# Optimization experiments

Measured on AMD Instinct MI355X. Metric: run time of the kernel, lower is better.

Reference implementation:

```python
import jax, jax.numpy as jnp
import numpy as np

C = 256
C8 = C // 8


def setup_inputs() -> dict:
    key = jax.random.key(0)
    ks = jax.random.split(key, 9)
    B, H, W = 4, 64, 64
    inp = jax.random.normal(ks[0], (B, C, H, W), dtype=jnp.float32)
    original = jax.random.normal(ks[1], (B, C, H, W), dtype=jnp.float32)
    s = 1.0 / np.sqrt(C)
    wq = jax.random.normal(ks[2], (C8, C), dtype=jnp.float32) * s
    bq = jax.random.normal(ks[3], (C8,), dtype=jnp.float32) * 0.01
    wk = jax.random.normal(ks[4], (C8, C), dtype=jnp.float32) * s
    bk = jax.random.normal(ks[5], (C8,), dtype=jnp.float32) * 0.01
    wv = jax.random.normal(ks[6], (C, C), dtype=jnp.float32) * s
    bv = jax.random.normal(ks[7], (C,), dtype=jnp.float32) * 0.01
    # torch inits gamma to 0; use a nonzero value so the attention branch contributes
    gamma = jnp.asarray([0.5], dtype=jnp.float32)
    return {"input": inp, "original": original, "wq": wq, "bq": bq,
            "wk": wk, "bk": bk, "wv": wv, "bv": bv, "gamma": gamma}


def reference(input, original, wq, bq, wk, bk, wv, bv, gamma):
    B, Cc, H, W = input.shape
    HW = H * W
    x = input.reshape(B, Cc, HW)          # [B, C, HW]
    o = original.reshape(B, Cc, HW)
    # 1x1 convs == per-pixel linear projections
    q = jnp.einsum('oc,bcn->bno', wq, x) + bq          # [B, HW, C8]
    k = jnp.einsum('oc,bcn->bon', wk, x) + bk[:, None]  # [B, C8, HW]
    v = jnp.einsum('oc,bcn->bon', wv, o) + bv[:, None]  # [B, C, HW]
    attn = jax.nn.softmax(jnp.einsum('bic,bcj->bij', q, k), axis=-1)  # [B, HW, HW]
    out = jnp.einsum('bcj,bij->bci', v, attn)           # [B, C, HW]
    out = out.reshape(B, Cc, H, W)
    return gamma[0] * out + input
```

## Files before the change

kernel.cpp:

```cpp
#include <hip/hip_runtime.h>

typedef short s16x8 __attribute__((ext_vector_type(8)));
typedef float f32x4 __attribute__((ext_vector_type(4)));
typedef float f32x16 __attribute__((ext_vector_type(16)));

#define B_ 4
#define C_ 256
#define S_ 4096
#define LOG2E 1.44269504088896f
#define M2 32.0f

#if __has_builtin(__builtin_amdgcn_exp2f)
#define EXP2(x) __builtin_amdgcn_exp2f(x)
#else
#define EXP2(x) __exp2f(x)
#endif

__device__ __forceinline__ unsigned short f2b(float f) {
  union { float f; unsigned u; } v; v.f = f;
  unsigned r = v.u + 0x7fffu + ((v.u >> 16) & 1u);
  return (unsigned short)(r >> 16);
}
__device__ __forceinline__ unsigned short f2b_fast(float f) {
  union { float f; unsigned u; } v; v.f = f;
  return (unsigned short)((v.u + 0x8000u) >> 16);
}
__device__ __forceinline__ s16x8 lds_ld8(const unsigned short* p) {
  union { s16x8 v; uint2 u[2]; } r;
  r.u[0] = *(const uint2*)p;
  r.u[1] = *(const uint2*)(p + 4);
  return r.v;
}

__global__ __launch_bounds__(256)
void proj_kernel(const float* __restrict__ x, const float* __restrict__ orig,
                 const float* __restrict__ wq, const float* __restrict__ bq,
                 const float* __restrict__ wk, const float* __restrict__ bk,
                 const float* __restrict__ wv, const float* __restrict__ bv,
                 unsigned short* __restrict__ Qb, unsigned short* __restrict__ Kb,
                 unsigned short* __restrict__ Vf) {
  __shared__ unsigned short Al[64 * 68];
  __shared__ unsigned short Sl[64 * 68];
  const int ct = blockIdx.x >> 6;
  const int jt = blockIdx.x & 63;
  const int n0 = jt * 64;
  const int b  = blockIdx.y;
  const int t  = threadIdx.x;
  const int L = t & 63, w = t >> 6;
  const int mt = w >> 1, nt = w & 1;
  const int g = L >> 5, l32 = L & 31;
  const float* srcb = ((ct == 0) ? x : orig) + (size_t)b * C_ * S_;
  f32x16 acc = (f32x16)0.0f;

  for (int kc = 0; kc < 4; ++kc) {
    const int k0 = kc * 64;
    __syncthreads();
    #pragma unroll
    for (int rep = 0; rep < 4; ++rep) {
      const int idx = rep * 256 + t;
      const int row = idx >> 4, c4 = (idx & 15) * 4;
      const float* wsrc; int wrow;
      if (ct == 0) {
        if (row < 32) { wsrc = wq; wrow = row; } else { wsrc = wk; wrow = row - 32; }
      } else { wsrc = wv; wrow = (ct - 1) * 64 + row; }
      f32x4 v = *(const f32x4*)(wsrc + (size_t)wrow * 256 + k0 + c4);
      union { unsigned short us[4]; uint2 u2; } pk;
      #pragma unroll
      for (int i = 0; i < 4; ++i) pk.us[i] = f2b(v[i]);
      *(uint2*)&Al[row * 68 + c4] = pk.u2;
    }
    {
      const int c4 = (t >> 4) * 4;
      const int n4 = (t & 15) * 4;
      f32x4 v0 = *(const f32x4*)(srcb + (size_t)(k0 + c4 + 0) * S_ + n0 + n4);
      f32x4 v1 = *(const f32x4*)(srcb + (size_t)(k0 + c4 + 1) * S_ + n0 + n4);
      f32x4 v2 = *(const f32x4*)(srcb + (size_t)(k0 + c4 + 2) * S_ + n0 + n4);
      f32x4 v3 = *(const f32x4*)(srcb + (size_t)(k0 + c4 + 3) * S_ + n0 + n4);
      #pragma unroll
      for (int k = 0; k < 4; ++k) {
        union { unsigned short us[4]; uint2 u2; } pk;
        pk.us[0] = f2b(v0[k]); pk.us[1] = f2b(v1[k]);
        pk.us[2] = f2b(v2[k]); pk.us[3] = f2b(v3[k]);
        *(uint2*)&Sl[(n4 + k) * 68 + c4] = pk.u2;
      }
    }
    __syncthreads();
    #pragma unroll
    for (int ks = 0; ks < 4; ++ks) {
      s16x8 af = lds_ld8(&Al[(mt * 32 + l32) * 68 + ks * 16 + g * 8]);
      s16x8 bf = lds_ld8(&Sl[(nt * 32 + l32) * 68 + ks * 16 + g * 8]);
      acc = __builtin_amdgcn_mfma_f32_32x32x16_bf16(af, bf, acc, 0, 0, 0);
    }
  }
  __syncthreads();
  unsigned short* Rl = Al;
  const int n = nt * 32 + l32;
  if (ct == 0) {
    #pragma unroll
    for (int reg = 0; reg < 16; ++reg) {
      const int rr = (reg & 3) + 8 * (reg >> 2) + 4 * g;
      const float val = (mt == 0) ? (acc[reg] + bq[rr]) * LOG2E : acc[reg] + bk[rr];
      Rl[n * 68 + mt * 32 + rr] = f2b(val);
    }
    __syncthreads();
    const int nn = t >> 2, ch0 = (t & 3) * 16;
    s16x8 a = lds_ld8(Rl + nn * 68 + ch0);
    s16x8 c = lds_ld8(Rl + nn * 68 + ch0 + 8);
    unsigned short* dst = (ch0 < 32)
        ? Qb + ((size_t)b * S_ + n0 + nn) * 32 + ch0
        : Kb + ((size_t)b * S_ + n0 + nn) * 32 + (ch0 - 32);
    *(s16x8*)dst = a;
    *(s16x8*)(dst + 8) = c;
  } else {
    const int cg = ct - 1;
    #pragma unroll
    for (int reg = 0; reg < 16; ++reg) {
      const int rr = (reg & 3) + 8 * (reg >> 2) + 4 * g;
      const int ch = mt * 32 + rr;
      Rl[ch * 68 + n] = f2b(acc[reg] + bv[cg * 64 + ch]);
    }
    __syncthreads();
    unsigned short* grp = Vf + ((size_t)(b * 64 + jt) * 4 + cg) * 4096;
    #pragma unroll
    for (int k = 0; k < 2; ++k) {
      const int G = t * 2 + k;
      const int vv = G >> 8, kb = (G >> 6) & 3, Lf = G & 63;
      const int ch64 = vv * 32 + (Lf & 31);
      const int j64  = kb * 16 + (Lf >> 5) * 8;
      s16x8 v = lds_ld8(Rl + ch64 * 68 + j64);
      *(s16x8*)(grp + G * 8) = v;
    }
  }
}

union FlashU {
  unsigned short P[64 * 68];
  float scr[128][66];
};

__global__ __launch_bounds__(512, 4)
void flash_kernel(const unsigned short* __restrict__ Qb,
                  const unsigned short* __restrict__ Kb,
                  const unsigned short* __restrict__ Vf,
                  const float* __restrict__ inp,
                  const float* __restrict__ gamma,
                  float* __restrict__ out) {
  __shared__ FlashU sm;
  __shared__ float lpart[2][64];
  __shared__ float invl[64];
  const int l   = blockIdx.x;
  const int b   = (l & 7) >> 1;
  const int chh = (l >> 3) & 1;
  const int i0  = ((l >> 4) * 2 + (l & 1)) * 64;
  const int t  = threadIdx.x;
  const int L = t & 63, w = t >> 6;
  const int q4 = L >> 4, c16 = L & 15;
  const int g  = L >> 5, l32 = L & 31;
  const int rh = w & 3, jh = w >> 2;
  const int cq = w & 3, ih = w >> 2;
  const float gam = gamma[0];
  const unsigned short* Kbase = Kb + (size_t)b * S_ * 32;
  const s16x8 qf = *(const s16x8*)(Qb + ((size_t)b * S_ + i0 + rh * 16 + c16) * 32 + q4 * 8);

  const int vcg = chh * 2 + (cq >> 1);
  const int vvv = cq & 1;

  f32x16 acc = (f32x16)0.0f;
  float lp[4] = {0.f, 0.f, 0.f, 0.f};

  s16x8 kc0 = *(const s16x8*)(Kbase + (size_t)(c16) * 32 + q4 * 8 + (size_t)(jh * 32) * 32);
  s16x8 kc1 = *(const s16x8*)(Kbase + (size_t)(jh * 32 + 16 + c16) * 32 + q4 * 8);

  for (int j0 = 0; j0 < S_; j0 += 64) {
    const int jt = j0 >> 6;
    const int jn = (j0 + 64 < S_) ? j0 + 64 : j0;
    s16x8 kn0 = *(const s16x8*)(Kbase + (size_t)(jn + jh * 32 + c16) * 32 + q4 * 8);
    s16x8 kn1 = *(const s16x8*)(Kbase + (size_t)(jn + jh * 32 + 16 + c16) * 32 + q4 * 8);
    const unsigned short* vb = Vf + ((size_t)(b * 64 + jt) * 4 + vcg) * 4096 + vvv * 2048;
    s16x8 vf0 = *(const s16x8*)(vb + 0 * 512 + L * 8);
    s16x8 vf1 = *(const s16x8*)(vb + 1 * 512 + L * 8);
    s16x8 vf2 = *(const s16x8*)(vb + 2 * 512 + L * 8);
    s16x8 vf3 = *(const s16x8*)(vb + 3 * 512 + L * 8);
    f32x4 cinit = (f32x4)(-M2);
    f32x4 s0 = __builtin_amdgcn_mfma_f32_16x16x32_bf16(qf, kc0, cinit, 0, 0, 0);
    f32x4 s1 = __builtin_amdgcn_mfma_f32_16x16x32_bf16(qf, kc1, cinit, 0, 0, 0);
    #pragma unroll
    for (int r = 0; r < 4; ++r) {
      const float p0 = EXP2(s0[r]);
      const float p1 = EXP2(s1[r]);
      lp[r] += p0 + p1;
      const int row = rh * 16 + q4 * 4 + r;
      sm.P[row * 68 + jh * 32 + c16]      = f2b_fast(p0);
      sm.P[row * 68 + jh * 32 + 16 + c16] = f2b_fast(p1);
    }
    __syncthreads();
    {
      s16x8 pf;
      pf = lds_ld8(sm.P + (ih * 32 + l32) * 68 + 0 * 16 + g * 8);
      acc = __builtin_amdgcn_mfma_f32_32x32x16_bf16(pf, vf0, acc, 0, 0, 0);
      pf = lds_ld8(sm.P + (ih * 32 + l32) * 68 + 1 * 16 + g * 8);
      acc = __builtin_amdgcn_mfma_f32_32x32x16_bf16(pf, vf1, acc, 0, 0, 0);
      pf = lds_ld8(sm.P + (ih * 32 + l32) * 68 + 2 * 16 + g * 8);
      acc = __builtin_amdgcn_mfma_f32_32x32x16_bf16(pf, vf2, acc, 0, 0, 0);
      pf = lds_ld8(sm.P + (ih * 32 + l32) * 68 + 3 * 16 + g * 8);
      acc = __builtin_amdgcn_mfma_f32_32x32x16_bf16(pf, vf3, acc, 0, 0, 0);
    }
    __syncthreads();
    kc0 = kn0; kc1 = kn1;
  }
  #pragma unroll
  for (int r = 0; r < 4; ++r) {
    float v = lp[r];
    #pragma unroll
    for (int d = 1; d < 16; d <<= 1) v += __shfl_xor(v, d, 64);
    lp[r] = v;
  }
  if (c16 == 0) {
    #pragma unroll
    for (int r = 0; r < 4; ++r) lpart[jh][rh * 16 + q4 * 4 + r] = lp[r];
  }
  __syncthreads();
  if (t < 64) invl[t] = gam / (lpart[0][t] + lpart[1][t]);
  #pragma unroll
  for (int reg = 0; reg < 16; ++reg) {
    const int rr = (reg & 3) + 8 * (reg >> 2) + 4 * g;
    sm.scr[cq * 32 + l32][ih * 32 + rr] = acc[reg];
  }
  __syncthreads();
  {
    const int ch = t >> 2;
    const int ic = (t & 3) * 16;
    #pragma unroll
    for (int q = 0; q < 4; ++q) {
      const int il = ic + q * 4;
      const size_t gi = ((size_t)b * C_ + chh * 128 + ch) * S_ + i0 + il;
      const f32x4 iv = *(const f32x4*)(inp + gi);
      f32x4 o;
      #pragma unroll
      for (int k = 0; k < 4; ++k)
        o[k] = sm.scr[ch][il + k] * invl[il + k] + iv[k];
      *(f32x4*)(out + gi) = o;
    }
  }
}

extern "C" void kernel_launch(void* const* d_in, const int* in_sizes, int n_in,
                              void* d_out, int out_size, void* d_ws, size_t ws_size,
                              hipStream_t stream) {
  const float* inp   = (const float*)d_in[0];
  const float* orig  = (const float*)d_in[1];
  const float* wq    = (const float*)d_in[2];
  const float* bq    = (const float*)d_in[3];
  const float* wk    = (const float*)d_in[4];
  const float* bk    = (const float*)d_in[5];
  const float* wv    = (const float*)d_in[6];
  const float* bv    = (const float*)d_in[7];
  const float* gamma = (const float*)d_in[8];
  float* out = (float*)d_out;

  unsigned short* Qb = (unsigned short*)d_ws;
  unsigned short* Kb = Qb + (size_t)B_ * S_ * 32;
  unsigned short* Vf = Kb + (size_t)B_ * S_ * 32;

  proj_kernel<<<dim3(320, 4), 256, 0, stream>>>(inp, orig, wq, bq, wk, bk, wv, bv, Qb, Kb, Vf);
  flash_kernel<<<512, 512, 0, stream>>>(Qb, Kb, Vf, inp, gamma, out);
}
```

Baseline: 168.4 us.

## Double-buffer P tile and software-pipeline flash loop with transposed score MFMA

The flash attention loop now uses two P buffers in LDS and is unrolled by two, so the exp/score phase of the next tile overlaps the PV MFMA of the current tile. This cuts the syncs per tile from two to one. The score MFMA operands are swapped (K as A, Q as B), so each lane holds four consecutive columns of one row. That allows packed 8-byte LDS stores and a single scalar row-sum reduced with two shuffles instead of sixteen. K/V loads are prefetched one tile further ahead, which raises register pressure and doubles P LDS usage.

```diff
diff --git a/kernel.cpp b/kernel.cpp
--- a/kernel.cpp
+++ b/kernel.cpp
@@ -134,9 +134,56 @@
 }
 
 union FlashU {
-  unsigned short P[64 * 68];
+  unsigned short P[2][64 * 68];
   float scr[128][66];
 };
+
+#define PHASE_A(PBUF, K0, K1)                                                   \
+  {                                                                             \
+    f32x4 cinit = (f32x4)(-M2);                                                 \
+    f32x4 s0 = __builtin_amdgcn_mfma_f32_16x16x32_bf16(K0, qf, cinit, 0, 0, 0); \
+    f32x4 s1 = __builtin_amdgcn_mfma_f32_16x16x32_bf16(K1, qf, cinit, 0, 0, 0); \
+    const float p0a = EXP2(s0[0]), p0b = EXP2(s0[1]);                           \
+    const float p0c = EXP2(s0[2]), p0d = EXP2(s0[3]);                           \
+    const float p1a = EXP2(s1[0]), p1b = EXP2(s1[1]);                           \
+    const float p1c = EXP2(s1[2]), p1d = EXP2(s1[3]);                           \
+    lpv += ((p0a + p0b) + (p0c + p0d)) + ((p1a + p1b) + (p1c + p1d));           \
+    uint2 w0, w1;                                                               \
+    w0.x = (unsigned)f2b_fast(p0a) | ((unsigned)f2b_fast(p0b) << 16);           \
+    w0.y = (unsigned)f2b_fast(p0c) | ((unsigned)f2b_fast(p0d) << 16);           \
+    w1.x = (unsigned)f2b_fast(p1a) | ((unsigned)f2b_fast(p1b) << 16);          \
+    w1.y = (unsigned)f2b_fast(p1c) | ((unsigned)f2b_fast(p1d) << 16);          \
+    unsigned short* pw = sm.P[PBUF] + prow_off;                                 \
+    *(uint2*)(pw)      = w0;                                                    \
+    *(uint2*)(pw + 16) = w1;                                                    \
+  }
+
+#define PHASE_B(PBUF, V0, V1, V2, V3)                                           \
+  {                                                                             \
+    s16x8 pf;                                                                   \
+    pf = lds_ld8(sm.P[PBUF] + pread_off + 0 * 16);                              \
+    acc = __builtin_amdgcn_mfma_f32_32x32x16_bf16(pf, V0, acc, 0, 0, 0);        \
+    pf = lds_ld8(sm.P[PBUF] + pread_off + 1 * 16);                              \
+    acc = __builtin_amdgcn_mfma_f32_32x32x16_bf16(pf, V1, acc, 0, 0, 0);        \
+    pf = lds_ld8(sm.P[PBUF] + pread_off + 2 * 16);                              \
+    acc = __builtin_amdgcn_mfma_f32_32x32x16_bf16(pf, V2, acc, 0, 0, 0);        \
+    pf = lds_ld8(sm.P[PBUF] + pread_off + 3 * 16);                              \
+    acc = __builtin_amdgcn_mfma_f32_32x32x16_bf16(pf, V3, acc, 0, 0, 0);        \
+  }
+
+#define LOAD_K(JT, K0, K1)                                                          \
+  K0 = *(const s16x8*)(Kbase + (size_t)((JT) * 64 + jh * 32 + c16) * 32 + q4 * 8);  \
+  K1 = *(const s16x8*)(Kbase + (size_t)((JT) * 64 + jh * 32 + 16 + c16) * 32 + q4 * 8);
+
+#define LOAD_V(JT, V0, V1, V2, V3)                                             \
+  {                                                                            \
+    const unsigned short* vb = Vf + ((size_t)(b * 64 + (JT)) * 4 + vcg) * 4096 \
+                               + vvv * 2048 + L * 8;                           \
+    V0 = *(const s16x8*)(vb + 0 * 512);                                        \
+    V1 = *(const s16x8*)(vb + 1 * 512);                                        \
+    V2 = *(const s16x8*)(vb + 2 * 512);                                        \
+    V3 = *(const s16x8*)(vb + 3 * 512);                                        \
+  }
 
 __global__ __launch_bounds__(512, 4)
 void flash_kernel(const unsigned short* __restrict__ Qb,
@@ -165,60 +212,35 @@
   const int vcg = chh * 2 + (cq >> 1);
   const int vvv = cq & 1;
 
+  const int prow_off  = (rh * 16 + c16) * 68 + jh * 32 + q4 * 4;
+  const int pread_off = (ih * 32 + l32) * 68 + g * 8;
+
   f32x16 acc = (f32x16)0.0f;
-  float lp[4] = {0.f, 0.f, 0.f, 0.f};
-
-  s16x8 kc0 = *(const s16x8*)(Kbase + (size_t)(c16) * 32 + q4 * 8 + (size_t)(jh * 32) * 32);
-  s16x8 kc1 = *(const s16x8*)(Kbase + (size_t)(jh * 32 + 16 + c16) * 32 + q4 * 8);
-
-  for (int j0 = 0; j0 < S_; j0 += 64) {
-    const int jt = j0 >> 6;
-    const int jn = (j0 + 64 < S_) ? j0 + 64 : j0;
-    s16x8 kn0 = *(const s16x8*)(Kbase + (size_t)(jn + jh * 32 + c16) * 32 + q4 * 8);
-    s16x8 kn1 = *(const s16x8*)(Kbase + (size_t)(jn + jh * 32 + 16 + c16) * 32 + q4 * 8);
-    const unsigned short* vb = Vf + ((size_t)(b * 64 + jt) * 4 + vcg) * 4096 + vvv * 2048;
-    s16x8 vf0 = *(const s16x8*)(vb + 0 * 512 + L * 8);
-    s16x8 vf1 = *(const s16x8*)(vb + 1 * 512 + L * 8);
-    s16x8 vf2 = *(const s16x8*)(vb + 2 * 512 + L * 8);
-    s16x8 vf3 = *(const s16x8*)(vb + 3 * 512 + L * 8);
-    f32x4 cinit = (f32x4)(-M2);
-    f32x4 s0 = __builtin_amdgcn_mfma_f32_16x16x32_bf16(qf, kc0, cinit, 0, 0, 0);
-    f32x4 s1 = __builtin_amdgcn_mfma_f32_16x16x32_bf16(qf, kc1, cinit, 0, 0, 0);
-    #pragma unroll
-    for (int r = 0; r < 4; ++r) {
-      const float p0 = EXP2(s0[r]);
-      const float p1 = EXP2(s1[r]);
-      lp[r] += p0 + p1;
-      const int row = rh * 16 + q4 * 4 + r;
-      sm.P[row * 68 + jh * 32 + c16]      = f2b_fast(p0);
-      sm.P[row * 68 + jh * 32 + 16 + c16] = f2b_fast(p1);
-    }
+  float lpv = 0.f;
+
+  s16x8 kE0, kE1, kO0, kO1;
+  s16x8 vE0, vE1, vE2, vE3, vO0, vO1, vO2, vO3;
+  LOAD_K(0, kE0, kE1);
+  LOAD_V(0, vE0, vE1, vE2, vE3);
+
+  for (int jt = 0; jt < 64; jt += 2) {
+    PHASE_A(0, kE0, kE1);
+    __syncthreads();
+    LOAD_K(jt + 1, kO0, kO1);
+    LOAD_V(jt + 1, vO0, vO1, vO2, vO3);
+    PHASE_B(0, vE0, vE1, vE2, vE3);
+    PHASE_A(1, kO0, kO1);
     __syncthreads();
     {
-      s16x8 pf;
-      pf = lds_ld8(sm.P + (ih * 32 + l32) * 68 + 0 * 16 + g * 8);
-      acc = __builtin_amdgcn_mfma_f32_32x32x16_bf16(pf, vf0, acc, 0, 0, 0);
-      pf = lds_ld8(sm.P + (ih * 32 + l32) * 68 + 1 * 16 + g * 8);
-      acc = __builtin_amdgcn_mfma_f32_32x32x16_bf16(pf, vf1, acc, 0, 0, 0);
-      pf = lds_ld8(sm.P + (ih * 32 + l32) * 68 + 2 * 16 + g * 8);
-      acc = __builtin_amdgcn_mfma_f32_32x32x16_bf16(pf, vf2, acc, 0, 0, 0);
-      pf = lds_ld8(sm.P + (ih * 32 + l32) * 68 + 3 * 16 + g * 8);
-      acc = __builtin_amdgcn_mfma_f32_32x32x16_bf16(pf, vf3, acc, 0, 0, 0);
-    }
-    __syncthreads();
-    kc0 = kn0; kc1 = kn1;
-  }
-  #pragma unroll
-  for (int r = 0; r < 4; ++r) {
-    float v = lp[r];
-    #pragma unroll
-    for (int d = 1; d < 16; d <<= 1) v += __shfl_xor(v, d, 64);
-    lp[r] = v;
-  }
-  if (c16 == 0) {
-    #pragma unroll
-    for (int r = 0; r < 4; ++r) lpart[jh][rh * 16 + q4 * 4 + r] = lp[r];
-  }
+      const int jn = (jt + 2 < 64) ? jt + 2 : 62;
+      LOAD_K(jn, kE0, kE1);
+      LOAD_V(jn, vE0, vE1, vE2, vE3);
+    }
+    PHASE_B(1, vO0, vO1, vO2, vO3);
+  }
+  lpv += __shfl_xor(lpv, 16, 64);
+  lpv += __shfl_xor(lpv, 32, 64);
+  if (L < 16) lpart[jh][rh * 16 + L] = lpv;
   __syncthreads();
   if (t < 64) invl[t] = gam / (lpart[0][t] + lpart[1][t]);
   #pragma unroll
```

Measured after the change: 172.8 us. 2.6% more time.

## Double-buffer P tile, process 128 keys per step with swapped QK operands

Applied to the files above, without the earlier changes.

The flash loop now handles 128 keys per iteration and ping-pongs between two P buffers in LDS. This cuts the barriers per key block from two to one and overlaps the PV MFMAs of one half with the softmax of the other. The QK MFMA operands are swapped so each lane owns one query row. That lets P be written as packed 4-element vector stores and the row-sum reduction drop to two shuffles. Two independent accumulators break the MFMA dependency chain, at the cost of more registers for K and V prefetches, which risks spills or lower occupancy under launch_bounds(512,4).

```diff
diff --git a/kernel.cpp b/kernel.cpp
--- a/kernel.cpp
+++ b/kernel.cpp
@@ -133,10 +133,79 @@
   }
 }
 
+#define PSTR 132
+
 union FlashU {
-  unsigned short P[64 * 68];
+  unsigned short P[2][64 * PSTR];
   float scr[128][66];
 };
+
+#define PACK4(S, DST)                                                           \
+  {                                                                             \
+    const float p0 = EXP2((S)[0]), p1 = EXP2((S)[1]);                           \
+    const float p2 = EXP2((S)[2]), p3 = EXP2((S)[3]);                           \
+    lpv += (p0 + p1) + (p2 + p3);                                               \
+    uint2 wv_;                                                                  \
+    wv_.x = (unsigned)f2b_fast(p0) | ((unsigned)f2b_fast(p1) << 16);            \
+    wv_.y = (unsigned)f2b_fast(p2) | ((unsigned)f2b_fast(p3) << 16);            \
+    *(uint2*)(DST) = wv_;                                                       \
+  }
+
+#define PHASE_A2(PBUF, KA, KB, KC, KD)                                          \
+  {                                                                             \
+    const f32x4 cinit = (f32x4)(-M2);                                           \
+    f32x4 s0 = __builtin_amdgcn_mfma_f32_16x16x32_bf16(KA, qf, cinit, 0, 0, 0); \
+    f32x4 s1 = __builtin_amdgcn_mfma_f32_16x16x32_bf16(KB, qf, cinit, 0, 0, 0); \
+    f32x4 s2 = __builtin_amdgcn_mfma_f32_16x16x32_bf16(KC, qf, cinit, 0, 0, 0); \
+    f32x4 s3 = __builtin_amdgcn_mfma_f32_16x16x32_bf16(KD, qf, cinit, 0, 0, 0); \
+    unsigned short* pw = sm.P[PBUF] + prowA;                                    \
+    PACK4(s0, pw);                                                              \
+    PACK4(s1, pw + 16);                                                         \
+    PACK4(s2, pw + 32);                                                         \
+    PACK4(s3, pw + 48);                                                         \
+  }
+
+#define PHASE_B2(PBUF)                                                          \
+  {                                                                             \
+    s16x8 pf;                                                                   \
+    pf = lds_ld8(sm.P[PBUF] + preadB + 0 * 16);                                 \
+    accA = __builtin_amdgcn_mfma_f32_32x32x16_bf16(pf, v0, accA, 0, 0, 0);      \
+    pf = lds_ld8(sm.P[PBUF] + preadB + 4 * 16);                                 \
+    accB = __builtin_amdgcn_mfma_f32_32x32x16_bf16(pf, v4, accB, 0, 0, 0);      \
+    pf = lds_ld8(sm.P[PBUF] + preadB + 1 * 16);                                 \
+    accA = __builtin_amdgcn_mfma_f32_32x32x16_bf16(pf, v1, accA, 0, 0, 0);      \
+    pf = lds_ld8(sm.P[PBUF] + preadB + 5 * 16);                                 \
+    accB = __builtin_amdgcn_mfma_f32_32x32x16_bf16(pf, v5, accB, 0, 0, 0);      \
+    pf = lds_ld8(sm.P[PBUF] + preadB + 2 * 16);                                 \
+    accA = __builtin_amdgcn_mfma_f32_32x32x16_bf16(pf, v2, accA, 0, 0, 0);      \
+    pf = lds_ld8(sm.P[PBUF] + preadB + 6 * 16);                                 \
+    accB = __builtin_amdgcn_mfma_f32_32x32x16_bf16(pf, v6, accB, 0, 0, 0);      \
+    pf = lds_ld8(sm.P[PBUF] + preadB + 3 * 16);                                 \
+    accA = __builtin_amdgcn_mfma_f32_32x32x16_bf16(pf, v3, accA, 0, 0, 0);      \
+    pf = lds_ld8(sm.P[PBUF] + preadB + 7 * 16);                                 \
+    accB = __builtin_amdgcn_mfma_f32_32x32x16_bf16(pf, v7, accB, 0, 0, 0);      \
+  }
+
+#define LOAD_K2(IU, KA, KB, KC, KD)                                                      \
+  KA = *(const s16x8*)(Kbase + (size_t)((IU) * 128 + jh * 64 +  0 + c16) * 32 + q4 * 8); \
+  KB = *(const s16x8*)(Kbase + (size_t)((IU) * 128 + jh * 64 + 16 + c16) * 32 + q4 * 8); \
+  KC = *(const s16x8*)(Kbase + (size_t)((IU) * 128 + jh * 64 + 32 + c16) * 32 + q4 * 8); \
+  KD = *(const s16x8*)(Kbase + (size_t)((IU) * 128 + jh * 64 + 48 + c16) * 32 + q4 * 8);
+
+#define LOAD_V2(IU)                                                                  \
+  {                                                                                  \
+    const unsigned short* vb0 = Vf + ((size_t)(b * 64 + (IU) * 2) * 4 + vcg) * 4096  \
+                                + vvv * 2048 + L * 8;                                \
+    v0 = *(const s16x8*)(vb0 + 0 * 512);                                             \
+    v1 = *(const s16x8*)(vb0 + 1 * 512);                                             \
+    v2 = *(const s16x8*)(vb0 + 2 * 512);                                             \
+    v3 = *(const s16x8*)(vb0 + 3 * 512);                                             \
+    const unsigned short* vb1 = vb0 + 4 * 4096;                                      \
+    v4 = *(const s16x8*)(vb1 + 0 * 512);                                             \
+    v5 = *(const s16x8*)(vb1 + 1 * 512);                                             \
+    v6 = *(const s16x8*)(vb1 + 2 * 512);                                             \
+    v7 = *(const s16x8*)(vb1 + 3 * 512);                                             \
+  }
 
 __global__ __launch_bounds__(512, 4)
 void flash_kernel(const unsigned short* __restrict__ Qb,
@@ -165,66 +234,44 @@
   const int vcg = chh * 2 + (cq >> 1);
   const int vvv = cq & 1;
 
-  f32x16 acc = (f32x16)0.0f;
-  float lp[4] = {0.f, 0.f, 0.f, 0.f};
-
-  s16x8 kc0 = *(const s16x8*)(Kbase + (size_t)(c16) * 32 + q4 * 8 + (size_t)(jh * 32) * 32);
-  s16x8 kc1 = *(const s16x8*)(Kbase + (size_t)(jh * 32 + 16 + c16) * 32 + q4 * 8);
-
-  for (int j0 = 0; j0 < S_; j0 += 64) {
-    const int jt = j0 >> 6;
-    const int jn = (j0 + 64 < S_) ? j0 + 64 : j0;
-    s16x8 kn0 = *(const s16x8*)(Kbase + (size_t)(jn + jh * 32 + c16) * 32 + q4 * 8);
-    s16x8 kn1 = *(const s16x8*)(Kbase + (size_t)(jn + jh * 32 + 16 + c16) * 32 + q4 * 8);
-    const unsigned short* vb = Vf + ((size_t)(b * 64 + jt) * 4 + vcg) * 4096 + vvv * 2048;
-    s16x8 vf0 = *(const s16x8*)(vb + 0 * 512 + L * 8);
-    s16x8 vf1 = *(const s16x8*)(vb + 1 * 512 + L * 8);
-    s16x8 vf2 = *(const s16x8*)(vb + 2 * 512 + L * 8);
-    s16x8 vf3 = *(const s16x8*)(vb + 3 * 512 + L * 8);
-    f32x4 cinit = (f32x4)(-M2);
-    f32x4 s0 = __builtin_amdgcn_mfma_f32_16x16x32_bf16(qf, kc0, cinit, 0, 0, 0);
-    f32x4 s1 = __builtin_amdgcn_mfma_f32_16x16x32_bf16(qf, kc1, cinit, 0, 0, 0);
-    #pragma unroll
-    for (int r = 0; r < 4; ++r) {
-      const float p0 = EXP2(s0[r]);
-      const float p1 = EXP2(s1[r]);
-      lp[r] += p0 + p1;
-      const int row = rh * 16 + q4 * 4 + r;
-      sm.P[row * 68 + jh * 32 + c16]      = f2b_fast(p0);
-      sm.P[row * 68 + jh * 32 + 16 + c16] = f2b_fast(p1);
-    }
+  const int prowA  = (rh * 16 + c16) * PSTR + jh * 64 + q4 * 4;
+  const int preadB = (ih * 32 + l32) * PSTR + g * 8;
+
+  f32x16 accA = (f32x16)0.0f, accB = (f32x16)0.0f;
+  float lpv = 0.f;
+
+  s16x8 kE0, kE1, kE2, kE3, kO0, kO1, kO2, kO3;
+  s16x8 v0, v1, v2, v3, v4, v5, v6, v7;
+  LOAD_K2(0, kE0, kE1, kE2, kE3);
+  LOAD_V2(0);
+
+  for (int u = 0; u < 32; u += 2) {
+    PHASE_A2(0, kE0, kE1, kE2, kE3);
+    __syncthreads();
+    LOAD_K2(u + 1, kO0, kO1, kO2, kO3);
+    PHASE_B2(0);
+    LOAD_V2(u + 1);
+    PHASE_A2(1, kO0, kO1, kO2, kO3);
     __syncthreads();
     {
-      s16x8 pf;
-      pf = lds_ld8(sm.P + (ih * 32 + l32) * 68 + 0 * 16 + g * 8);
-      acc = __builtin_amdgcn_mfma_f32_32x32x16_bf16(pf, vf0, acc, 0, 0, 0);
-      pf = lds_ld8(sm.P + (ih * 32 + l32) * 68 + 1 * 16 + g * 8);
-      acc = __builtin_amdgcn_mfma_f32_32x32x16_bf16(pf, vf1, acc, 0, 0, 0);
-      pf = lds_ld8(sm.P + (ih * 32 + l32) * 68 + 2 * 16 + g * 8);
-      acc = __builtin_amdgcn_mfma_f32_32x32x16_bf16(pf, vf2, acc, 0, 0, 0);
-      pf = lds_ld8(sm.P + (ih * 32 + l32) * 68 + 3 * 16 + g * 8);
-      acc = __builtin_amdgcn_mfma_f32_32x32x16_bf16(pf, vf3, acc, 0, 0, 0);
-    }
-    __syncthreads();
-    kc0 = kn0; kc1 = kn1;
-  }
-  #pragma unroll
-  for (int r = 0; r < 4; ++r) {
-    float v = lp[r];
-    #pragma unroll
-    for (int d = 1; d < 16; d <<= 1) v += __shfl_xor(v, d, 64);
-    lp[r] = v;
-  }
-  if (c16 == 0) {
-    #pragma unroll
-    for (int r = 0; r < 4; ++r) lpart[jh][rh * 16 + q4 * 4 + r] = lp[r];
-  }
+      const int un = (u + 2 < 32) ? u + 2 : 31;
+      LOAD_K2(un, kE0, kE1, kE2, kE3);
+    }
+    PHASE_B2(1);
+    {
+      const int un = (u + 2 < 32) ? u + 2 : 31;
+      LOAD_V2(un);
+    }
+  }
+  lpv += __shfl_xor(lpv, 16, 64);
+  lpv += __shfl_xor(lpv, 32, 64);
+  if (L < 16) lpart[jh][rh * 16 + L] = lpv;
   __syncthreads();
   if (t < 64) invl[t] = gam / (lpart[0][t] + lpart[1][t]);
   #pragma unroll
   for (int reg = 0; reg < 16; ++reg) {
     const int rr = (reg & 3) + 8 * (reg >> 2) + 4 * g;
-    sm.scr[cq * 32 + l32][ih * 32 + rr] = acc[reg];
+    sm.scr[cq * 32 + l32][ih * 32 + rr] = accA[reg] + accB[reg];
   }
   __syncthreads();
   {
```

Measured after the change: 172.7 us. 1.03x slower.

## Keep P in registers via transposed S=K·Q MFMA and split keys across waves

Applied to the files above, without the earlier changes.

Restructures the flash kernel so each wave computes S^T with 32x32 MFMAs (K as A operand). The exponentiated scores are then packed straight into registers as the B-operand layout for the P·V MFMAs, removing the per-tile LDS round trip and both __syncthreads in the main loop. Waves split the key dimension into four quarters, and each block now covers all 256 channels for 64 queries, so the grid is halved. Partial accumulators are merged through serialized LDS adds at the end. V's workspace layout in the projection kernel is changed to match. The cost is much higher register pressure (eight 16-wide accumulators, launch bounds lowered to 2), a larger LDS reduction buffer, and a serialized epilogue.

```diff
diff --git a/kernel.cpp b/kernel.cpp
--- a/kernel.cpp
+++ b/kernel.cpp
@@ -25,6 +25,7 @@
   union { float f; unsigned u; } v; v.f = f;
   return (unsigned short)((v.u + 0x8000u) >> 16);
 }
+#define PK2(x, y) ((unsigned)f2b_fast(x) | ((unsigned)f2b_fast(y) << 16))
 __device__ __forceinline__ s16x8 lds_ld8(const unsigned short* p) {
   union { s16x8 v; uint2 u[2]; } r;
   r.u[0] = *(const uint2*)p;
@@ -120,125 +121,156 @@
       Rl[ch * 68 + n] = f2b(acc[reg] + bv[cg * 64 + ch]);
     }
     __syncthreads();
-    unsigned short* grp = Vf + ((size_t)(b * 64 + jt) * 4 + cg) * 4096;
     #pragma unroll
     for (int k = 0; k < 2; ++k) {
       const int G = t * 2 + k;
-      const int vv = G >> 8, kb = (G >> 6) & 3, Lf = G & 63;
-      const int ch64 = vv * 32 + (Lf & 31);
-      const int j64  = kb * 16 + (Lf >> 5) * 8;
-      s16x8 v = lds_ld8(Rl + ch64 * 68 + j64);
-      *(s16x8*)(grp + G * 8) = v;
-    }
-  }
-}
-
-union FlashU {
-  unsigned short P[64 * 68];
-  float scr[128][66];
-};
-
-__global__ __launch_bounds__(512, 4)
+      const int t2 = G >> 8;
+      const int gh = (G >> 7) & 1;
+      const int s  = (G >> 6) & 1;
+      const int Lf = G & 63;
+      const int hh = Lf >> 5;
+      const int ch_l = gh * 32 + (Lf & 31);
+      const int jloc = t2 * 32 + s * 16 + hh * 4;
+      uint2 q0 = *(const uint2*)&Rl[ch_l * 68 + jloc];
+      uint2 q1 = *(const uint2*)&Rl[ch_l * 68 + jloc + 8];
+      unsigned short* dst = Vf + (((size_t)(b * 128 + jt * 2 + t2) * 8)
+                                  + cg * 2 + gh) * 1024 + s * 512 + (size_t)Lf * 8;
+      *(uint2*)dst = q0;
+      *(uint2*)(dst + 4) = q1;
+    }
+  }
+}
+
+
+#define MFMA32(A, B, C) __builtin_amdgcn_mfma_f32_32x32x16_bf16(A, B, C, 0, 0, 0)
+
+#define LOADV(JT)                                                               \
+  {                                                                             \
+    const unsigned short* vb = Vf + (((size_t)(b * 128 + (JT)) * 8)             \
+                                     + chh * 4) * 1024 + (size_t)L * 8;         \
+    v00 = *(const s16x8*)(vb + 0 * 1024);                                       \
+    v01 = *(const s16x8*)(vb + 0 * 1024 + 512);                                 \
+    v10 = *(const s16x8*)(vb + 1 * 1024);                                       \
+    v11 = *(const s16x8*)(vb + 1 * 1024 + 512);                                 \
+    v20 = *(const s16x8*)(vb + 2 * 1024);                                       \
+    v21 = *(const s16x8*)(vb + 2 * 1024 + 512);                                 \
+    v30 = *(const s16x8*)(vb + 3 * 1024);                                       \
+    v31 = *(const s16x8*)(vb + 3 * 1024 + 512);                                 \
+  }
+
+#define DO_IG(QF0, QF1, A0, A1, A2, A3, LPV)                                    \
+  {                                                                             \
+    f32x16 p = MFMA32(kc0, QF0, cinit);                                         \
+    p = MFMA32(kc1, QF1, p);                                                    \
+    const float e0 = EXP2(p[0]),  e1 = EXP2(p[1]),  e2 = EXP2(p[2]),  e3 = EXP2(p[3]);   \
+    const float e4 = EXP2(p[4]),  e5 = EXP2(p[5]),  e6 = EXP2(p[6]),  e7 = EXP2(p[7]);   \
+    const float e8 = EXP2(p[8]),  e9 = EXP2(p[9]),  e10 = EXP2(p[10]), e11 = EXP2(p[11]); \
+    const float e12 = EXP2(p[12]), e13 = EXP2(p[13]), e14 = EXP2(p[14]), e15 = EXP2(p[15]); \
+    LPV += (((e0 + e1) + (e2 + e3)) + ((e4 + e5) + (e6 + e7)))                  \
+         + (((e8 + e9) + (e10 + e11)) + ((e12 + e13) + (e14 + e15)));           \
+    union { unsigned u[4]; s16x8 v; } pa, pb;                                   \
+    pa.u[0] = PK2(e0, e1);   pa.u[1] = PK2(e2, e3);                             \
+    pa.u[2] = PK2(e4, e5);   pa.u[3] = PK2(e6, e7);                             \
+    pb.u[0] = PK2(e8, e9);   pb.u[1] = PK2(e10, e11);                           \
+    pb.u[2] = PK2(e12, e13); pb.u[3] = PK2(e14, e15);                           \
+    A0 = MFMA32(pa.v, v00, A0);  A0 = MFMA32(pb.v, v01, A0);                    \
+    A1 = MFMA32(pa.v, v10, A1);  A1 = MFMA32(pb.v, v11, A1);                    \
+    A2 = MFMA32(pa.v, v20, A2);  A2 = MFMA32(pb.v, v21, A2);                    \
+    A3 = MFMA32(pa.v, v30, A3);  A3 = MFMA32(pb.v, v31, A3);                    \
+  }
+
+#define DUMP_ADD(ACC, IG, CG)                                                   \
+  _Pragma("unroll")                                                             \
+  for (int r = 0; r < 16; ++r) {                                                \
+    const int rr = (r & 3) + 8 * (r >> 2) + 4 * h;                              \
+    scr[(IG) * 32 + rr][chh * 128 + (CG) * 32 + l31] += ACC[r];                 \
+  }
+
+__global__ __launch_bounds__(512, 2)
 void flash_kernel(const unsigned short* __restrict__ Qb,
                   const unsigned short* __restrict__ Kb,
                   const unsigned short* __restrict__ Vf,
                   const float* __restrict__ inp,
                   const float* __restrict__ gamma,
                   float* __restrict__ out) {
-  __shared__ FlashU sm;
-  __shared__ float lpart[2][64];
+  __shared__ float scr[64][260];
+  __shared__ float lpart[4][64];
   __shared__ float invl[64];
-  const int l   = blockIdx.x;
-  const int b   = (l & 7) >> 1;
-  const int chh = (l >> 3) & 1;
-  const int i0  = ((l >> 4) * 2 + (l & 1)) * 64;
+  const int l  = blockIdx.x;
+  const int b  = (l & 7) >> 1;
+  const int i0 = ((l >> 3) * 2 + (l & 1)) * 64;
   const int t  = threadIdx.x;
   const int L = t & 63, w = t >> 6;
-  const int q4 = L >> 4, c16 = L & 15;
-  const int g  = L >> 5, l32 = L & 31;
-  const int rh = w & 3, jh = w >> 2;
-  const int cq = w & 3, ih = w >> 2;
+  const int l31 = L & 31, h = L >> 5;
+  const int jq = w >> 1, chh = w & 1;
   const float gam = gamma[0];
   const unsigned short* Kbase = Kb + (size_t)b * S_ * 32;
-  const s16x8 qf = *(const s16x8*)(Qb + ((size_t)b * S_ + i0 + rh * 16 + c16) * 32 + q4 * 8);
-
-  const int vcg = chh * 2 + (cq >> 1);
-  const int vvv = cq & 1;
-
-  f32x16 acc = (f32x16)0.0f;
-  float lp[4] = {0.f, 0.f, 0.f, 0.f};
-
-  s16x8 kc0 = *(const s16x8*)(Kbase + (size_t)(c16) * 32 + q4 * 8 + (size_t)(jh * 32) * 32);
-  s16x8 kc1 = *(const s16x8*)(Kbase + (size_t)(jh * 32 + 16 + c16) * 32 + q4 * 8);
-
-  for (int j0 = 0; j0 < S_; j0 += 64) {
-    const int jt = j0 >> 6;
-    const int jn = (j0 + 64 < S_) ? j0 + 64 : j0;
-    s16x8 kn0 = *(const s16x8*)(Kbase + (size_t)(jn + jh * 32 + c16) * 32 + q4 * 8);
-    s16x8 kn1 = *(const s16x8*)(Kbase + (size_t)(jn + jh * 32 + 16 + c16) * 32 + q4 * 8);
-    const unsigned short* vb = Vf + ((size_t)(b * 64 + jt) * 4 + vcg) * 4096 + vvv * 2048;
-    s16x8 vf0 = *(const s16x8*)(vb + 0 * 512 + L * 8);
-    s16x8 vf1 = *(const s16x8*)(vb + 1 * 512 + L * 8);
-    s16x8 vf2 = *(const s16x8*)(vb + 2 * 512 + L * 8);
-    s16x8 vf3 = *(const s16x8*)(vb + 3 * 512 + L * 8);
-    f32x4 cinit = (f32x4)(-M2);
-    f32x4 s0 = __builtin_amdgcn_mfma_f32_16x16x32_bf16(qf, kc0, cinit, 0, 0, 0);
-    f32x4 s1 = __builtin_amdgcn_mfma_f32_16x16x32_bf16(qf, kc1, cinit, 0, 0, 0);
-    #pragma unroll
-    for (int r = 0; r < 4; ++r) {
-      const float p0 = EXP2(s0[r]);
-      const float p1 = EXP2(s1[r]);
-      lp[r] += p0 + p1;
-      const int row = rh * 16 + q4 * 4 + r;
-      sm.P[row * 68 + jh * 32 + c16]      = f2b_fast(p0);
-      sm.P[row * 68 + jh * 32 + 16 + c16] = f2b_fast(p1);
-    }
-    __syncthreads();
+
+  {
+    float* sf = &scr[0][0];
+    for (int z = t; z < 64 * 260; z += 512) sf[z] = 0.0f;
+  }
+
+  const s16x8 qf00 = *(const s16x8*)(Qb + ((size_t)b * S_ + i0 + l31) * 32 + h * 8);
+  const s16x8 qf01 = *(const s16x8*)(Qb + ((size_t)b * S_ + i0 + l31) * 32 + 16 + h * 8);
+  const s16x8 qf10 = *(const s16x8*)(Qb + ((size_t)b * S_ + i0 + 32 + l31) * 32 + h * 8);
+  const s16x8 qf11 = *(const s16x8*)(Qb + ((size_t)b * S_ + i0 + 32 + l31) * 32 + 16 + h * 8);
+
+  f32x16 a00 = (f32x16)0.0f, a01 = (f32x16)0.0f, a02 = (f32x16)0.0f, a03 = (f32x16)0.0f;
+  f32x16 a10 = (f32x16)0.0f, a11 = (f32x16)0.0f, a12 = (f32x16)0.0f, a13 = (f32x16)0.0f;
+  float lp0 = 0.f, lp1 = 0.f;
+  const f32x16 cinit = (f32x16)(-M2);
+
+  s16x8 kc0, kc1, kn0, kn1;
+  s16x8 v00, v01, v10, v11, v20, v21, v30, v31;
+  {
+    const int jt0 = jq * 32;
+    kc0 = *(const s16x8*)(Kbase + (size_t)(jt0 * 32 + l31) * 32 + h * 8);
+    kc1 = *(const s16x8*)(Kbase + (size_t)(jt0 * 32 + l31) * 32 + 16 + h * 8);
+  }
+
+  for (int st = 0; st < 32; ++st) {
+    const int jt = jq * 32 + st;
+    LOADV(jt);
+    DO_IG(qf00, qf01, a00, a01, a02, a03, lp0);
     {
-      s16x8 pf;
-      pf = lds_ld8(sm.P + (ih * 32 + l32) * 68 + 0 * 16 + g * 8);
-      acc = __builtin_amdgcn_mfma_f32_32x32x16_bf16(pf, vf0, acc, 0, 0, 0);
-      pf = lds_ld8(sm.P + (ih * 32 + l32) * 68 + 1 * 16 + g * 8);
-      acc = __builtin_amdgcn_mfma_f32_32x32x16_bf16(pf, vf1, acc, 0, 0, 0);
-      pf = lds_ld8(sm.P + (ih * 32 + l32) * 68 + 2 * 16 + g * 8);
-      acc = __builtin_amdgcn_mfma_f32_32x32x16_bf16(pf, vf2, acc, 0, 0, 0);
-      pf = lds_ld8(sm.P + (ih * 32 + l32) * 68 + 3 * 16 + g * 8);
-      acc = __builtin_amdgcn_mfma_f32_32x32x16_bf16(pf, vf3, acc, 0, 0, 0);
-    }
-    __syncthreads();
+      const int jn = (jt + 1 < 128) ? jt + 1 : 127;
+      kn0 = *(const s16x8*)(Kbase + (size_t)(jn * 32 + l31) * 32 + h * 8);
+      kn1 = *(const s16x8*)(Kbase + (size_t)(jn * 32 + l31) * 32 + 16 + h * 8);
+    }
+    DO_IG(qf10, qf11, a10, a11, a12, a13, lp1);
     kc0 = kn0; kc1 = kn1;
   }
-  #pragma unroll
-  for (int r = 0; r < 4; ++r) {
-    float v = lp[r];
-    #pragma unroll
-    for (int d = 1; d < 16; d <<= 1) v += __shfl_xor(v, d, 64);
-    lp[r] = v;
-  }
-  if (c16 == 0) {
-    #pragma unroll
-    for (int r = 0; r < 4; ++r) lpart[jh][rh * 16 + q4 * 4 + r] = lp[r];
+
+  lp0 += __shfl_xor(lp0, 32, 64);
+  lp1 += __shfl_xor(lp1, 32, 64);
+  if (chh == 0 && L < 32) {
+    lpart[jq][L] = lp0;
+    lpart[jq][32 + L] = lp1;
+  }
+  #pragma unroll 1
+  for (int ph = 0; ph < 4; ++ph) {
+    __syncthreads();
+    if (jq == ph) {
+      DUMP_ADD(a00, 0, 0); DUMP_ADD(a01, 0, 1); DUMP_ADD(a02, 0, 2); DUMP_ADD(a03, 0, 3);
+      DUMP_ADD(a10, 1, 0); DUMP_ADD(a11, 1, 1); DUMP_ADD(a12, 1, 2); DUMP_ADD(a13, 1, 3);
+    }
   }
   __syncthreads();
-  if (t < 64) invl[t] = gam / (lpart[0][t] + lpart[1][t]);
-  #pragma unroll
-  for (int reg = 0; reg < 16; ++reg) {
-    const int rr = (reg & 3) + 8 * (reg >> 2) + 4 * g;
-    sm.scr[cq * 32 + l32][ih * 32 + rr] = acc[reg];
-  }
+  if (t < 64) invl[t] = gam / (lpart[0][t] + lpart[1][t] + lpart[2][t] + lpart[3][t]);
   __syncthreads();
   {
-    const int ch = t >> 2;
-    const int ic = (t & 3) * 16;
-    #pragma unroll
-    for (int q = 0; q < 4; ++q) {
-      const int il = ic + q * 4;
-      const size_t gi = ((size_t)b * C_ + chh * 128 + ch) * S_ + i0 + il;
+    const int ch = t >> 1;
+    const int ih = (t & 1) * 32;
+    #pragma unroll
+    for (int q = 0; q < 8; ++q) {
+      const int il = ih + q * 4;
+      const size_t gi = ((size_t)b * C_ + ch) * S_ + i0 + il;
       const f32x4 iv = *(const f32x4*)(inp + gi);
       f32x4 o;
       #pragma unroll
       for (int k = 0; k < 4; ++k)
-        o[k] = sm.scr[ch][il + k] * invl[il + k] + iv[k];
+        o[k] = scr[il + k][ch] * invl[il + k] + iv[k];
       *(f32x4*)(out + gi) = o;
     }
   }
@@ -263,5 +295,5 @@
   unsigned short* Vf = Kb + (size_t)B_ * S_ * 32;
 
   proj_kernel<<<dim3(320, 4), 256, 0, stream>>>(inp, orig, wq, bq, wk, bk, wv, bv, Qb, Kb, Vf);
-  flash_kernel<<<512, 512, 0, stream>>>(Qb, Kb, Vf, inp, gamma, out);
-}
+  flash_kernel<<<256, 512, 0, stream>>>(Qb, Kb, Vf, inp, gamma, out);
+}
```

Result: faster. 158.0 us (median of 3 runs) (-6.2%).
